# Performance work log

Measured on AMD Instinct MI355X. Metric: run time of the kernel, lower is better.

The kernel has to match this reference:

```python
import jax, jax.numpy as jnp
import numpy as np

EMBED_DIM = 1024
NUM_HEADS = 16
HEAD_DIM = EMBED_DIM // NUM_HEADS


def setup_inputs() -> dict:
    key = jax.random.key(0)
    ks = jax.random.split(key, 9)
    B, S, E, hd = 2, 2048, EMBED_DIM, HEAD_DIM
    s_e = 1.0 / np.sqrt(E)
    return {
        "x": jax.random.normal(ks[0], (B, S, E), dtype=jnp.float32),
        "wq": jax.random.uniform(ks[1], (E, E), jnp.float32, -s_e, s_e),
        "bq": jax.random.uniform(ks[2], (E,), jnp.float32, -s_e, s_e),
        "wk": jax.random.uniform(ks[3], (E, hd), jnp.float32, -s_e, s_e),
        "bk": jax.random.uniform(ks[4], (hd,), jnp.float32, -s_e, s_e),
        "wv": jax.random.uniform(ks[5], (E, hd), jnp.float32, -s_e, s_e),
        "bv": jax.random.uniform(ks[6], (hd,), jnp.float32, -s_e, s_e),
        "wo": jax.random.uniform(ks[7], (E, E), jnp.float32, -s_e, s_e),
        "bo": jax.random.uniform(ks[8], (E,), jnp.float32, -s_e, s_e),
    }


def reference(x, wq, bq, wk, bk, wv, bv, wo, bo):
    B, S, E = x.shape
    H, hd = NUM_HEADS, HEAD_DIM
    # projections
    q = (x @ wq + bq).reshape(B, S, H, hd)          # [B,S,H,hd]
    k = x @ wk + bk                                  # [B,S,hd] shared across heads
    v = x @ wv + bv                                  # [B,S,hd]
    scale = 1.0 / np.sqrt(hd).astype(np.float32)
    # scores: [B,H,S_q,S_k]
    scores = jnp.einsum('bqhd,bkd->bhqk', q, k) * scale
    attn = jax.nn.softmax(scores, axis=-1)
    out = jnp.einsum('bhqk,bkd->bqhd', attn, v).reshape(B, S, E)
    return out @ wo + bo
```

## Files before the change

### kernel.cpp

```cpp
#include <hip/hip_runtime.h>
#include <stdint.h>

#define SLEN 2048
#define EDIM 1024
#define NH 16
#define HD 64
#define QLD 1152

typedef unsigned short u16;
typedef short bf8 __attribute__((ext_vector_type(8)));
typedef float f4 __attribute__((ext_vector_type(4)));
typedef bf8 bf8_a __attribute__((may_alias));
typedef uint2 uint2_a __attribute__((may_alias));
typedef uint4 uint4_a __attribute__((may_alias));
typedef float4 float4_a __attribute__((may_alias));

__device__ __forceinline__ float bf2f(u16 u) {
  union { unsigned u; float f; } c; c.u = ((unsigned)u) << 16; return c.f;
}
__device__ __forceinline__ u16 f2bf(float x) {
  union { __bf16 h; u16 u; } c; c.h = (__bf16)x; return c.u;
}
__device__ __forceinline__ unsigned pk2bf(float a, float b) {
  union { __bf16 h[2]; unsigned u; } c;
  c.h[0] = (__bf16)a; c.h[1] = (__bf16)b;
  return c.u;
}
__device__ __forceinline__ void async_cp16(u16* lds, const u16* g) {
  __builtin_amdgcn_global_load_lds((__attribute__((address_space(1))) void*)g,
                                   (__attribute__((address_space(3))) void*)lds,
                                   16, 0, 0);
}

__device__ __forceinline__ void tcvt_tile(const float* src, int srcLd,
                                          u16* dst, int dstLd, int r0, int c0) {
  __shared__ u16 tile[64][65];
  const int t = threadIdx.x;
#pragma unroll
  for (int i = 0; i < 16; ++i) {
    int e = i * 256 + t, rr = e >> 6, cc = e & 63;
    tile[rr][cc] = f2bf(src[(size_t)(r0 + rr) * srcLd + c0 + cc]);
  }
  __syncthreads();
#pragma unroll
  for (int i = 0; i < 16; ++i) {
    int e = i * 256 + t, j = e >> 6, ii = e & 63;
    dst[(size_t)(c0 + j) * dstLd + r0 + ii] = tile[ii][j];
  }
}

__global__ void prep_w(const float* wq, const float* wk, const float* wv,
                       const float* wo, const float* bq, const float* bk,
                       const float* bv, const float* bo,
                       u16* wT, u16* woT, float* bQKV, float* bOut) {
  const int yy = blockIdx.y;
  if (yy < 16) tcvt_tile(wq, 1024, wT, 1024, blockIdx.x * 64, yy * 64);
  else if (yy < 32) tcvt_tile(wo, 1024, woT, 1024, blockIdx.x * 64, (yy - 16) * 64);
  else if (yy == 32) tcvt_tile(wk, 64, wT + (size_t)1024 * 1024, 1024, blockIdx.x * 64, 0);
  else if (yy == 33) tcvt_tile(wv, 64, wT + (size_t)1088 * 1024, 1024, blockIdx.x * 64, 0);
  else {
    int i = blockIdx.x * 256 + threadIdx.x;
    if (i < 1024) bQKV[i] = bq[i];
    else if (i < 1088) bQKV[i] = bk[i - 1024];
    else if (i < 1152) bQKV[i] = bv[i - 1088];
    int j = i - 1152;
    if (j >= 0 && j < 1024) bOut[j] = bo[j];
  }
}

__global__ __launch_bounds__(256) void gemm_qkv(
    const float* __restrict__ X, const u16* __restrict__ Bt,
    const float* __restrict__ bias, u16* __restrict__ C,
    u16* __restrict__ vtb) {
  __shared__ __align__(16) u16 As[64 * 64];
  __shared__ __align__(16) u16 Bs[128 * 64];
  const int K = 1024;
  const int tn0 = blockIdx.x * 128, tm0 = blockIdx.y * 64;
  const int tid = threadIdx.x, wave = tid >> 6, lane = tid & 63;
  const int quad = lane >> 4, l16 = lane & 15;
  const int wm = wave & 1, wn = wave >> 1;

  f4 acc[2][4];
#pragma unroll
  for (int i = 0; i < 2; ++i)
#pragma unroll
    for (int j = 0; j < 4; ++j) acc[i][j] = f4{0.f, 0.f, 0.f, 0.f};

  int aslot[2], bslot[4]; size_t aoff[2], boff[4];
#pragma unroll
  for (int i = 0; i < 2; ++i) {
    int s = i * 256 + tid, m = s >> 3, kc = s & 7, c = (kc - m) & 7;
    aslot[i] = s; aoff[i] = (size_t)(tm0 + m) * K + c * 8;
  }
#pragma unroll
  for (int i = 0; i < 4; ++i) {
    int s = i * 256 + tid, n = s >> 3, kc = s & 7, c = (kc - n) & 7;
    bslot[i] = s; boff[i] = (size_t)(tn0 + n) * K + c * 8;
  }
  int ard[2][2], brd[4][2];
#pragma unroll
  for (int mi = 0; mi < 2; ++mi) {
    int m = wm * 32 + mi * 16 + l16;
#pragma unroll
    for (int kk = 0; kk < 2; ++kk)
      ard[mi][kk] = (m * 8 + (((kk * 4 + quad) + m) & 7)) * 8;
  }
#pragma unroll
  for (int ni = 0; ni < 4; ++ni) {
    int n = wn * 64 + ni * 16 + l16;
#pragma unroll
    for (int kk = 0; kk < 2; ++kk)
      brd[ni][kk] = (n * 8 + (((kk * 4 + quad) + n) & 7)) * 8;
  }

  for (int it = 0; it < 16; ++it) {
    const size_t kb = (size_t)it * 64;
    uint4 staged[2];
#pragma unroll
    for (int i = 0; i < 2; ++i) {
      float4 f0 = *(const float4_a*)(X + aoff[i] + kb);
      float4 f1 = *(const float4_a*)(X + aoff[i] + kb + 4);
      staged[i].x = pk2bf(f0.x, f0.y);
      staged[i].y = pk2bf(f0.z, f0.w);
      staged[i].z = pk2bf(f1.x, f1.y);
      staged[i].w = pk2bf(f1.z, f1.w);
    }
    __syncthreads();
#pragma unroll
    for (int i = 0; i < 2; ++i) *(uint4_a*)&As[aslot[i] * 8] = staged[i];
#pragma unroll
    for (int i = 0; i < 4; ++i) async_cp16(&Bs[bslot[i] * 8], Bt + boff[i] + kb);
    __syncthreads();
#pragma unroll
    for (int kk = 0; kk < 2; ++kk) {
      bf8 af[2], bfr[4];
#pragma unroll
      for (int mi = 0; mi < 2; ++mi) af[mi] = *(const bf8_a*)&As[ard[mi][kk]];
#pragma unroll
      for (int ni = 0; ni < 4; ++ni) bfr[ni] = *(const bf8_a*)&Bs[brd[ni][kk]];
#pragma unroll
      for (int mi = 0; mi < 2; ++mi)
#pragma unroll
        for (int ni = 0; ni < 4; ++ni)
          acc[mi][ni] = __builtin_amdgcn_mfma_f32_16x16x32_bf16(
              af[mi], bfr[ni], acc[mi][ni], 0, 0, 0);
    }
  }

  float bv[4];
#pragma unroll
  for (int ni = 0; ni < 4; ++ni) bv[ni] = bias[tn0 + wn * 64 + ni * 16 + l16];
#pragma unroll
  for (int mi = 0; mi < 2; ++mi) {
    int row0 = tm0 + wm * 32 + mi * 16 + quad * 4;
#pragma unroll
    for (int ni = 0; ni < 4; ++ni) {
      int col = tn0 + wn * 64 + ni * 16 + l16;
      float vv[4];
#pragma unroll
      for (int r = 0; r < 4; ++r) vv[r] = acc[mi][ni][r] + bv[ni];
#pragma unroll
      for (int r = 0; r < 4; ++r)
        C[(size_t)(row0 + r) * QLD + col] = f2bf(vv[r]);
      if (col >= 1088) {
        int d = col - 1088, bb = row0 >> 11, s0 = row0 & 2047;
        uint2 pk;
        pk.x = pk2bf(vv[0], vv[1]);
        pk.y = pk2bf(vv[2], vv[3]);
        *(uint2_a*)&vtb[(size_t)(bb * 64 + d) * SLEN + s0] = pk;
      }
    }
  }
}

__global__ __launch_bounds__(128, 6) void attn_kernel(
    const u16* __restrict__ qkv, const u16* __restrict__ vT,
    u16* __restrict__ Opart, float* __restrict__ lpart) {
  __shared__ __align__(16) u16 Kf[4096];
  __shared__ __align__(16) u16 Vf[4096];
  __shared__ __align__(16) u16 Ps[2048];
  const int qt = blockIdx.x, bh = blockIdx.y, ks = blockIdx.z;
  const int b = bh >> 4, h = bh & 15;
  const int tid = threadIdx.x, wave = tid >> 6, lane = tid & 63;
  const int quad = lane >> 4, l16 = lane & 15;

#pragma unroll
  for (int i = 0; i < 4; ++i) {
    int d = i * 128 + tid;
    int kk = d >> 8, g = (d >> 6) & 3, qd = (d >> 4) & 3, r16 = d & 15;
    u16* dst = (kk == 0) ? &Kf[d * 8] : &Vf[(d - 256) * 8];
    async_cp16(dst, qkv + (size_t)(b * SLEN + qt * 64 + g * 16 + r16) * QLD +
                        h * HD + (kk * 4 + qd) * 8);
  }
  __syncthreads();
  bf8 bq[2][2];
#pragma unroll
  for (int nt = 0; nt < 2; ++nt) {
    bq[nt][0] = *(const bf8_a*)&Kf[((wave * 2 + nt) * 64 + lane) * 8];
    bq[nt][1] = *(const bf8_a*)&Vf[((wave * 2 + nt) * 64 + lane) * 8];
  }

  f4 acc_o[2][4];
#pragma unroll
  for (int i = 0; i < 2; ++i)
#pragma unroll
    for (int j = 0; j < 4; ++j) acc_o[i][j] = f4{0.f, 0.f, 0.f, 0.f};
  f4 lr4[2] = {f4{0.f, 0.f, 0.f, 0.f}, f4{0.f, 0.f, 0.f, 0.f}};
  const float C1 = 0.125f * 1.44269504089f;
  const int psb = wave * 1024;

  for (int kt = ks * 16; kt < ks * 16 + 16; ++kt) {
    __syncthreads();
#pragma unroll
    for (int i = 0; i < 4; ++i) {
      int d = i * 128 + tid;
      int kk = d >> 8, kg = (d >> 6) & 3, qd = (d >> 4) & 3, r16 = d & 15;
      async_cp16(&Kf[d * 8],
                 qkv + (size_t)(b * SLEN + kt * 64 + kg * 16 + r16) * QLD +
                     EDIM + (kk * 4 + qd) * 8);
    }
#pragma unroll
    for (int i = 0; i < 4; ++i) {
      int d = i * 128 + tid;
      int k4 = d >> 8, ni = (d >> 6) & 3, qd = (d >> 4) & 3, r16 = d & 15;
      async_cp16(&Vf[d * 8],
                 vT + (size_t)(b * 64 + ni * 16 + r16) * SLEN + kt * 64 +
                     (k4 * 4 + qd) * 8);
    }
    __syncthreads();

#pragma unroll
    for (int k4 = 0; k4 < 2; ++k4) {
      f4 st[2][2];
#pragma unroll
      for (int j = 0; j < 2; ++j)
#pragma unroll
        for (int nt = 0; nt < 2; ++nt) st[j][nt] = f4{0.f, 0.f, 0.f, 0.f};
#pragma unroll
      for (int kk = 0; kk < 2; ++kk)
#pragma unroll
        for (int j = 0; j < 2; ++j) {
          bf8 ak = *(const bf8_a*)&Kf[((kk * 4 + k4 * 2 + j) * 64 + lane) * 8];
#pragma unroll
          for (int nt = 0; nt < 2; ++nt)
            st[j][nt] = __builtin_amdgcn_mfma_f32_16x16x32_bf16(
                ak, bq[nt][kk], st[j][nt], 0, 0, 0);
        }
#pragma unroll
      for (int nt = 0; nt < 2; ++nt)
#pragma unroll
        for (int j = 0; j < 2; ++j) {
          f4 pe;
          pe[0] = __builtin_amdgcn_exp2f(st[j][nt][0] * C1);
          pe[1] = __builtin_amdgcn_exp2f(st[j][nt][1] * C1);
          pe[2] = __builtin_amdgcn_exp2f(st[j][nt][2] * C1);
          pe[3] = __builtin_amdgcn_exp2f(st[j][nt][3] * C1);
          lr4[nt] += pe;
          uint2 pk;
          pk.x = pk2bf(pe[0], pe[1]);
          pk.y = pk2bf(pe[2], pe[3]);
          int qd2 = j * 2 + (quad >> 1);
          *(uint2_a*)&Ps[psb + ((nt * 4 + qd2) * 16 + l16) * 8 + (quad & 1) * 4] = pk;
        }
      asm volatile("" ::: "memory");
      bf8 ap[2];
#pragma unroll
      for (int mt = 0; mt < 2; ++mt)
        ap[mt] = *(const bf8_a*)&Ps[psb + ((mt * 4 + quad) * 16 + l16) * 8];
#pragma unroll
      for (int ni = 0; ni < 4; ++ni) {
        bf8 bv = *(const bf8_a*)&Vf[((k4 * 4 + ni) * 64 + lane) * 8];
#pragma unroll
        for (int mt = 0; mt < 2; ++mt)
          acc_o[mt][ni] = __builtin_amdgcn_mfma_f32_16x16x32_bf16(
              ap[mt], bv, acc_o[mt][ni], 0, 0, 0);
      }
      asm volatile("" ::: "memory");
    }
  }

  const size_t pbase = (size_t)(ks * 32 + bh) * 2048 + qt * 64;
  float ls[2];
#pragma unroll
  for (int nt = 0; nt < 2; ++nt) {
    float s = (lr4[nt][0] + lr4[nt][1]) + (lr4[nt][2] + lr4[nt][3]);
    s += __shfl_xor(s, 16, 64);
    s += __shfl_xor(s, 32, 64);
    ls[nt] = s;
    if (quad == 0) lpart[pbase + wave * 32 + nt * 16 + l16] = s;
  }
#pragma unroll
  for (int mt = 0; mt < 2; ++mt)
#pragma unroll
    for (int r = 0; r < 4; ++r) {
      size_t row = pbase + wave * 32 + mt * 16 + quad * 4 + r;
#pragma unroll
      for (int ni = 0; ni < 4; ++ni)
        Opart[row * 64 + ni * 16 + l16] = f2bf(acc_o[mt][ni][r]);
    }
}

__global__ __launch_bounds__(256) void gemm_out(
    const u16* __restrict__ Op, const float* __restrict__ lp,
    const u16* __restrict__ Bt, const float* __restrict__ bias,
    float* __restrict__ C) {
  __shared__ __align__(16) u16 As[64 * 64];
  __shared__ __align__(16) u16 Bs[128 * 64];
  const int K = 1024;
  const int tn0 = blockIdx.x * 128, tm0 = blockIdx.y * 64;
  const int tid = threadIdx.x, wave = tid >> 6, lane = tid & 63;
  const int quad = lane >> 4, l16 = lane & 15;
  const int wm = wave & 1, wn = wave >> 1;

  f4 acc[2][4];
#pragma unroll
  for (int i = 0; i < 2; ++i)
#pragma unroll
    for (int j = 0; j < 4; ++j) acc[i][j] = f4{0.f, 0.f, 0.f, 0.f};

  int aslot[2]; size_t obase[2]; int lbase[2];
#pragma unroll
  for (int i = 0; i < 2; ++i) {
    int s = i * 256 + tid, m = s >> 3, kc = s & 7, c = (kc - m) & 7;
    aslot[i] = s;
    int rowg = tm0 + m, b = rowg >> 11, qrow = rowg & 2047;
    obase[i] = (size_t)b * 2097152 + (size_t)qrow * 64 + c * 8;
    lbase[i] = b * 32768 + qrow;
  }
  int bslot[4]; size_t boff[4];
#pragma unroll
  for (int i = 0; i < 4; ++i) {
    int s = i * 256 + tid, n = s >> 3, kc = s & 7, c = (kc - n) & 7;
    bslot[i] = s; boff[i] = (size_t)(tn0 + n) * K + c * 8;
  }
  int ard[2][2], brd[4][2];
#pragma unroll
  for (int mi = 0; mi < 2; ++mi) {
    int m = wm * 32 + mi * 16 + l16;
#pragma unroll
    for (int kk = 0; kk < 2; ++kk)
      ard[mi][kk] = (m * 8 + (((kk * 4 + quad) + m) & 7)) * 8;
  }
#pragma unroll
  for (int ni = 0; ni < 4; ++ni) {
    int n = wn * 64 + ni * 16 + l16;
#pragma unroll
    for (int kk = 0; kk < 2; ++kk)
      brd[ni][kk] = (n * 8 + (((kk * 4 + quad) + n) & 7)) * 8;
  }

  for (int it = 0; it < 16; ++it) {
    uint4 staged[2];
#pragma unroll
    for (int i = 0; i < 2; ++i) {
      uint4 a0 = *(const uint4_a*)(Op + obase[i] + (size_t)it * 131072);
      uint4 a1 = *(const uint4_a*)(Op + obase[i] + (size_t)it * 131072 + 4194304);
      float l0 = lp[lbase[i] + it * 2048];
      float l1 = lp[lbase[i] + 65536 + it * 2048];
      float inv = 1.f / (l0 + l1);
      const u16* pa = (const u16*)&a0;
      const u16* pb = (const u16*)&a1;
      u16 tmp[8];
#pragma unroll
      for (int j = 0; j < 8; ++j)
        tmp[j] = f2bf((bf2f(pa[j]) + bf2f(pb[j])) * inv);
      staged[i] = *(const uint4_a*)tmp;
    }
    __syncthreads();
#pragma unroll
    for (int i = 0; i < 2; ++i) *(uint4_a*)&As[aslot[i] * 8] = staged[i];
#pragma unroll
    for (int i = 0; i < 4; ++i)
      async_cp16(&Bs[bslot[i] * 8], Bt + boff[i] + (size_t)it * 64);
    __syncthreads();
#pragma unroll
    for (int kk = 0; kk < 2; ++kk) {
      bf8 af[2], bfr[4];
#pragma unroll
      for (int mi = 0; mi < 2; ++mi) af[mi] = *(const bf8_a*)&As[ard[mi][kk]];
#pragma unroll
      for (int ni = 0; ni < 4; ++ni) bfr[ni] = *(const bf8_a*)&Bs[brd[ni][kk]];
#pragma unroll
      for (int mi = 0; mi < 2; ++mi)
#pragma unroll
        for (int ni = 0; ni < 4; ++ni)
          acc[mi][ni] = __builtin_amdgcn_mfma_f32_16x16x32_bf16(
              af[mi], bfr[ni], acc[mi][ni], 0, 0, 0);
    }
  }

  float bv[4];
#pragma unroll
  for (int ni = 0; ni < 4; ++ni) bv[ni] = bias[tn0 + wn * 64 + ni * 16 + l16];
#pragma unroll
  for (int mi = 0; mi < 2; ++mi) {
    int row0 = tm0 + wm * 32 + mi * 16 + quad * 4;
#pragma unroll
    for (int ni = 0; ni < 4; ++ni) {
      int col = tn0 + wn * 64 + ni * 16 + l16;
#pragma unroll
      for (int r = 0; r < 4; ++r)
        C[(size_t)(row0 + r) * 1024 + col] = acc[mi][ni][r] + bv[ni];
    }
  }
}

extern "C" void kernel_launch(void* const* d_in, const int* in_sizes, int n_in,
                              void* d_out, int out_size, void* d_ws, size_t ws_size,
                              hipStream_t stream) {
  const float* x  = (const float*)d_in[0];
  const float* wq = (const float*)d_in[1];
  const float* bq = (const float*)d_in[2];
  const float* wk = (const float*)d_in[3];
  const float* bk = (const float*)d_in[4];
  const float* wv = (const float*)d_in[5];
  const float* bv = (const float*)d_in[6];
  const float* wo = (const float*)d_in[7];
  const float* bo = (const float*)d_in[8];

  char* ws = (char*)d_ws;
  size_t off = 0;
  auto carve = [&](size_t bytes) {
    void* p = ws + off;
    off = (off + bytes + 255) & ~(size_t)255;
    return p;
  };
  u16* wT      = (u16*)carve((size_t)1152 * 1024 * 2);
  u16* woT     = (u16*)carve((size_t)1024 * 1024 * 2);
  float* bQKV  = (float*)carve(1152 * 4);
  float* bOut  = (float*)carve(1024 * 4);
  u16* qkvb    = (u16*)carve((size_t)4096 * QLD * 2);
  u16* vTb     = (u16*)carve((size_t)2 * 64 * SLEN * 2);
  u16* Opart   = (u16*)carve((size_t)2 * 32 * 2048 * 64 * 2);
  float* lpart = (float*)carve((size_t)2 * 32 * 2048 * 4);

  prep_w<<<dim3(16, 35), 256, 0, stream>>>(wq, wk, wv, wo, bq, bk, bv, bo,
                                           wT, woT, bQKV, bOut);

  gemm_qkv<<<dim3(9, 64), 256, 0, stream>>>(x, wT, bQKV, qkvb, vTb);

  attn_kernel<<<dim3(32, 32, 2), 128, 0, stream>>>(qkvb, vTb, Opart, lpart);

  gemm_out<<<dim3(8, 64), 256, 0, stream>>>(Opart, lpart, woT, bOut,
                                            (float*)d_out);
}
```

Baseline: 216.9 us.

## Enlarge attention tiles to 128 queries/keys and split keys four ways

The attention kernel now uses 256-thread blocks that each process 128 query rows against 128-key tiles. The key dimension is split into four partitions instead of two, so each block runs 4 iterations instead of 16. The output GEMM now reduces four partial outputs and denominators instead of two. The goal is to reuse each K/V tile across more queries and cut per-tile sync overhead. The cost is more partial-output traffic, more LDS per block and lower occupancy.

```diff
diff --git a/kernel.cpp b/kernel.cpp
--- a/kernel.cpp
+++ b/kernel.cpp
@@ -173,12 +173,12 @@
   }
 }
 
-__global__ __launch_bounds__(128, 6) void attn_kernel(
+__global__ __launch_bounds__(256, 4) void attn_kernel(
     const u16* __restrict__ qkv, const u16* __restrict__ vT,
     u16* __restrict__ Opart, float* __restrict__ lpart) {
-  __shared__ __align__(16) u16 Kf[4096];
-  __shared__ __align__(16) u16 Vf[4096];
-  __shared__ __align__(16) u16 Ps[2048];
+  __shared__ __align__(16) u16 Kf[8192];
+  __shared__ __align__(16) u16 Vf[8192];
+  __shared__ __align__(16) u16 Ps[4096];
   const int qt = blockIdx.x, bh = blockIdx.y, ks = blockIdx.z;
   const int b = bh >> 4, h = bh & 15;
   const int tid = threadIdx.x, wave = tid >> 6, lane = tid & 63;
@@ -186,19 +186,19 @@
 
 #pragma unroll
   for (int i = 0; i < 4; ++i) {
-    int d = i * 128 + tid;
-    int kk = d >> 8, g = (d >> 6) & 3, qd = (d >> 4) & 3, r16 = d & 15;
-    u16* dst = (kk == 0) ? &Kf[d * 8] : &Vf[(d - 256) * 8];
-    async_cp16(dst, qkv + (size_t)(b * SLEN + qt * 64 + g * 16 + r16) * QLD +
-                        h * HD + (kk * 4 + qd) * 8);
+    int d = i * 256 + tid;
+    int kk = d >> 9, g = (d >> 6) & 7, qd = (d >> 4) & 3, r16 = d & 15;
+    async_cp16(&Kf[d * 8],
+               qkv + (size_t)(b * SLEN + qt * 128 + g * 16 + r16) * QLD +
+                   h * HD + (kk * 4 + qd) * 8);
   }
   __syncthreads();
   bf8 bq[2][2];
 #pragma unroll
-  for (int nt = 0; nt < 2; ++nt) {
-    bq[nt][0] = *(const bf8_a*)&Kf[((wave * 2 + nt) * 64 + lane) * 8];
-    bq[nt][1] = *(const bf8_a*)&Vf[((wave * 2 + nt) * 64 + lane) * 8];
-  }
+  for (int nt = 0; nt < 2; ++nt)
+#pragma unroll
+    for (int kk = 0; kk < 2; ++kk)
+      bq[nt][kk] = *(const bf8_a*)&Kf[((kk * 8 + wave * 2 + nt) * 64 + lane) * 8];
 
   f4 acc_o[2][4];
 #pragma unroll
@@ -209,28 +209,28 @@
   const float C1 = 0.125f * 1.44269504089f;
   const int psb = wave * 1024;
 
-  for (int kt = ks * 16; kt < ks * 16 + 16; ++kt) {
+  for (int kt = ks * 4; kt < ks * 4 + 4; ++kt) {
     __syncthreads();
 #pragma unroll
     for (int i = 0; i < 4; ++i) {
-      int d = i * 128 + tid;
-      int kk = d >> 8, kg = (d >> 6) & 3, qd = (d >> 4) & 3, r16 = d & 15;
+      int d = i * 256 + tid;
+      int kk = d >> 9, k8 = (d >> 6) & 7, qd = (d >> 4) & 3, r16 = d & 15;
       async_cp16(&Kf[d * 8],
-                 qkv + (size_t)(b * SLEN + kt * 64 + kg * 16 + r16) * QLD +
+                 qkv + (size_t)(b * SLEN + kt * 128 + k8 * 16 + r16) * QLD +
                      EDIM + (kk * 4 + qd) * 8);
     }
 #pragma unroll
     for (int i = 0; i < 4; ++i) {
-      int d = i * 128 + tid;
+      int d = i * 256 + tid;
       int k4 = d >> 8, ni = (d >> 6) & 3, qd = (d >> 4) & 3, r16 = d & 15;
       async_cp16(&Vf[d * 8],
-                 vT + (size_t)(b * 64 + ni * 16 + r16) * SLEN + kt * 64 +
+                 vT + (size_t)(b * 64 + ni * 16 + r16) * SLEN + kt * 128 +
                      (k4 * 4 + qd) * 8);
     }
     __syncthreads();
 
 #pragma unroll
-    for (int k4 = 0; k4 < 2; ++k4) {
+    for (int k4 = 0; k4 < 4; ++k4) {
       f4 st[2][2];
 #pragma unroll
       for (int j = 0; j < 2; ++j)
@@ -240,7 +240,7 @@
       for (int kk = 0; kk < 2; ++kk)
 #pragma unroll
         for (int j = 0; j < 2; ++j) {
-          bf8 ak = *(const bf8_a*)&Kf[((kk * 4 + k4 * 2 + j) * 64 + lane) * 8];
+          bf8 ak = *(const bf8_a*)&Kf[((kk * 8 + k4 * 2 + j) * 64 + lane) * 8];
 #pragma unroll
           for (int nt = 0; nt < 2; ++nt)
             st[j][nt] = __builtin_amdgcn_mfma_f32_16x16x32_bf16(
@@ -279,7 +279,7 @@
     }
   }
 
-  const size_t pbase = (size_t)(ks * 32 + bh) * 2048 + qt * 64;
+  const size_t pbase = (size_t)((ks * 32 + bh) * 16 + qt) * 128;
   float ls[2];
 #pragma unroll
   for (int nt = 0; nt < 2; ++nt) {
@@ -353,17 +353,22 @@
     uint4 staged[2];
 #pragma unroll
     for (int i = 0; i < 2; ++i) {
-      uint4 a0 = *(const uint4_a*)(Op + obase[i] + (size_t)it * 131072);
-      uint4 a1 = *(const uint4_a*)(Op + obase[i] + (size_t)it * 131072 + 4194304);
-      float l0 = lp[lbase[i] + it * 2048];
-      float l1 = lp[lbase[i] + 65536 + it * 2048];
-      float inv = 1.f / (l0 + l1);
-      const u16* pa = (const u16*)&a0;
-      const u16* pb = (const u16*)&a1;
+      uint4 ap[4];
+      float lsum = 0.f;
+#pragma unroll
+      for (int p = 0; p < 4; ++p) {
+        ap[p] = *(const uint4_a*)(Op + obase[i] + (size_t)it * 131072 +
+                                  (size_t)p * 4194304);
+        lsum += lp[lbase[i] + it * 2048 + p * 65536];
+      }
+      float inv = 1.f / lsum;
       u16 tmp[8];
 #pragma unroll
-      for (int j = 0; j < 8; ++j)
-        tmp[j] = f2bf((bf2f(pa[j]) + bf2f(pb[j])) * inv);
+      for (int j = 0; j < 8; ++j) {
+        float s = bf2f(((const u16*)&ap[0])[j]) + bf2f(((const u16*)&ap[1])[j]) +
+                  bf2f(((const u16*)&ap[2])[j]) + bf2f(((const u16*)&ap[3])[j]);
+        tmp[j] = f2bf(s * inv);
+      }
       staged[i] = *(const uint4_a*)tmp;
     }
     __syncthreads();
@@ -431,15 +436,15 @@
   float* bOut  = (float*)carve(1024 * 4);
   u16* qkvb    = (u16*)carve((size_t)4096 * QLD * 2);
   u16* vTb     = (u16*)carve((size_t)2 * 64 * SLEN * 2);
-  u16* Opart   = (u16*)carve((size_t)2 * 32 * 2048 * 64 * 2);
-  float* lpart = (float*)carve((size_t)2 * 32 * 2048 * 4);
+  u16* Opart   = (u16*)carve((size_t)4 * 32 * 16 * 128 * 64 * 2);
+  float* lpart = (float*)carve((size_t)4 * 32 * 16 * 128 * 4);
 
   prep_w<<<dim3(16, 35), 256, 0, stream>>>(wq, wk, wv, wo, bq, bk, bv, bo,
                                            wT, woT, bQKV, bOut);
 
   gemm_qkv<<<dim3(9, 64), 256, 0, stream>>>(x, wT, bQKV, qkvb, vTb);
 
-  attn_kernel<<<dim3(32, 32, 2), 128, 0, stream>>>(qkvb, vTb, Opart, lpart);
+  attn_kernel<<<dim3(16, 32, 4), 256, 0, stream>>>(qkvb, vTb, Opart, lpart);
 
   gemm_out<<<dim3(8, 64), 256, 0, stream>>>(Opart, lpart, woT, bOut,
                                             (float*)d_out);
```

New measurement: 228.0 us. 1.05x slower.
